# Kernel optimization log

Measured on AMD Instinct MI355X. Metric: run time of the kernel, lower is better.

Reference implementation:

```python
import jax, jax.numpy as jnp
import numpy as np


def setup_inputs() -> dict:
    key = jax.random.key(0)
    ks = jax.random.split(key, 6)
    B_, S, D_in, D_out, R, NH = 4, 2048, 4096, 4096, 16, 8
    return {
        "x": jax.random.normal(ks[0], (B_, S, D_in), dtype=jnp.float32),
        "W": jax.random.normal(ks[1], (D_out, D_in), dtype=jnp.float32) * 0.02,
        "b": jax.random.normal(ks[2], (D_out,), dtype=jnp.float32) * 0.02,
        "A": jax.random.normal(ks[3], (NH, R, D_in), dtype=jnp.float32) * 0.02,
        "H_mat": jax.random.normal(ks[4], (NH, R, R), dtype=jnp.float32) * 0.02,
        "B": jax.random.normal(ks[5], (NH, D_out, R), dtype=jnp.float32) * 0.02,
        "s": jnp.ones((NH,), dtype=jnp.float32),
    }


def reference(x, W, b, A, H_mat, B, s):
    # base linear: [B,S,D_out]
    out = jnp.einsum("bsd,od->bso", x, W) + b
    # batched low-rank adapter chain over heads h:
    # ax  = x @ A[h].T    : [B,h,S,r]
    ax = jnp.einsum("bsd,hrd->bhsr", x, A)
    # hax = ax @ H[h].T   : [B,h,S,r]
    hax = jnp.einsum("bhsr,hqr->bhsq", ax, H_mat)
    # accumulate s[h] * (hax @ B[h].T) into out
    out = out + jnp.einsum("h,bhsq,hoq->bso", s, hax, B)
    return out
```

## Files before the change

### kernel.cpp

```cpp
#include <hip/hip_runtime.h>
#include <hip/hip_bf16.h>

typedef __attribute__((ext_vector_type(4))) float f32x4;
typedef __attribute__((ext_vector_type(8))) short bf16x8;

#define M_DIM 8192
#define N_DIM 4096
#define K_DIM 4096
#define NH 8
#define R_DIM 16
#define HQ 128

__device__ __forceinline__ unsigned short f2bf(float f) {
  union { float f; unsigned int u; } v; v.f = f;
  unsigned int r = v.u + 0x7fffu + ((v.u >> 16) & 1u);
  return (unsigned short)(r >> 16);
}

__device__ __forceinline__ void gll16(const void* gptr, void* lptr) {
  __builtin_amdgcn_global_load_lds(
      (const __attribute__((address_space(1))) void*)gptr,
      (__attribute__((address_space(3))) void*)lptr, 16, 0, 0);
}

__device__ __forceinline__ unsigned lds_addr(const void* p) {
  return (unsigned)(uintptr_t)(const __attribute__((address_space(3))) void*)p;
}

#define FENCE() asm volatile("" ::: "memory")
#define BAR() do { FENCE(); __builtin_amdgcn_s_barrier(); FENCE(); } while (0)
#define LGKM(N) do { asm volatile("s_waitcnt lgkmcnt(" #N ")" ::: "memory"); \
  __builtin_amdgcn_sched_barrier(0); } while (0)
#define VMC(N) asm volatile("s_waitcnt vmcnt(" #N ")" ::: "memory")
#define DSR(D, ADDR, IMM) asm volatile("ds_read_b128 %0, %1 offset:%2" \
  : "=&v"(D) : "v"(ADDR), "i"(IMM))

__global__ void k_cast_bf16(const float* __restrict__ in,
                            unsigned short* __restrict__ out, int n4) {
  int i = blockIdx.x * 256 + threadIdx.x;
  if (i >= n4) return;
  float4 v = reinterpret_cast<const float4*>(in)[i];
  ushort4 o;
  o.x = f2bf(v.x); o.y = f2bf(v.y); o.z = f2bf(v.z); o.w = f2bf(v.w);
  reinterpret_cast<ushort4*>(out)[i] = o;
}

__global__ void k_ha_t(const float* __restrict__ A, const float* __restrict__ H,
                       const float* __restrict__ s, unsigned short* __restrict__ HA_T) {
  const int d = blockIdx.x * 256 + threadIdx.x;
  const int h = blockIdx.y;
  const float* Ah = A + (size_t)h * R_DIM * K_DIM;
  const float* Hh = H + h * R_DIM * R_DIM;
  const float sv = s[h];
  float acc[R_DIM];
  #pragma unroll
  for (int q = 0; q < R_DIM; ++q) acc[q] = 0.f;
  #pragma unroll
  for (int r = 0; r < R_DIM; ++r) {
    float a = Ah[(size_t)r * K_DIM + d];
    #pragma unroll
    for (int q = 0; q < R_DIM; ++q) acc[q] += Hh[q * R_DIM + r] * a;
  }
  unsigned short o[R_DIM];
  #pragma unroll
  for (int q = 0; q < R_DIM; ++q) o[q] = f2bf(acc[q] * sv);
  *reinterpret_cast<uint4*>(&HA_T[(size_t)d * HQ + h * R_DIM]) = *reinterpret_cast<uint4*>(o);
  *reinterpret_cast<uint4*>(&HA_T[(size_t)d * HQ + h * R_DIM + 8]) = *reinterpret_cast<uint4*>(o + 8);
}

__global__ void k_bcat(const float* __restrict__ Bm, unsigned short* __restrict__ Bc) {
  const int t = threadIdx.x;
  const int ol = t >> 4, q = t & 15;
  const int o = blockIdx.x * 16 + ol;
  #pragma unroll
  for (int h = 0; h < NH; ++h)
    Bc[(size_t)o * HQ + h * R_DIM + q] = f2bf(Bm[((size_t)h * N_DIM + o) * R_DIM + q]);
}

__global__ __launch_bounds__(256)
void k_weff_mfma(const unsigned short* __restrict__ Ab,
                 const unsigned short* __restrict__ Bb,
                 const float* __restrict__ W,
                 unsigned short* __restrict__ Weff) {
  constexpr int WK = HQ;
  __shared__ unsigned short As[128 * 32];
  __shared__ unsigned short Bs[128 * 32];

  const int t = threadIdx.x;
  const int lane = t & 63;
  const int wave = t >> 6;
  const int wr = wave >> 1, wc = wave & 1;
  const int brow = blockIdx.y * 128;
  const int bcol = blockIdx.x * 128;

  const int r0 = t >> 2, ch = t & 3;
  const size_t a_off0 = (size_t)(brow + r0) * WK + ch * 8;
  const size_t a_off1 = (size_t)(brow + r0 + 64) * WK + ch * 8;
  const size_t b_off0 = (size_t)(bcol + r0) * WK + ch * 8;
  const size_t b_off1 = (size_t)(bcol + r0 + 64) * WK + ch * 8;
  unsigned short* as_d0 = As + t * 8;
  unsigned short* as_d1 = As + (t + 256) * 8;
  unsigned short* bs_d0 = Bs + t * 8;
  unsigned short* bs_d1 = Bs + (t + 256) * 8;

  const int fr = lane & 15;
  const int kk = (lane >> 4) * 8;

  f32x4 acc[4][4] = {};

  for (int k0 = 0; k0 < WK; k0 += 32) {
    gll16(Ab + a_off0 + k0, as_d0);
    gll16(Ab + a_off1 + k0, as_d1);
    gll16(Bb + b_off0 + k0, bs_d0);
    gll16(Bb + b_off1 + k0, bs_d1);
    __syncthreads();

    bf16x8 af[4], bfr[4];
    #pragma unroll
    for (int m = 0; m < 4; ++m)
      af[m] = *reinterpret_cast<const bf16x8*>(&As[(wr * 64 + m * 16 + fr) * 32 + kk]);
    #pragma unroll
    for (int n = 0; n < 4; ++n)
      bfr[n] = *reinterpret_cast<const bf16x8*>(&Bs[(wc * 64 + n * 16 + fr) * 32 + kk]);

    #pragma unroll
    for (int m = 0; m < 4; ++m)
      #pragma unroll
      for (int n = 0; n < 4; ++n)
        acc[m][n] = __builtin_amdgcn_mfma_f32_16x16x32_bf16(af[m], bfr[n], acc[m][n], 0, 0, 0);

    __syncthreads();
  }

  const int crow0 = brow + wr * 64 + (lane >> 4) * 4;
  const int ccol0 = bcol + wc * 64 + fr;
  #pragma unroll
  for (int m = 0; m < 4; ++m)
    #pragma unroll
    for (int n = 0; n < 4; ++n) {
      const int col = ccol0 + n * 16;
      #pragma unroll
      for (int r = 0; r < 4; ++r) {
        const size_t idx = (size_t)(crow0 + m * 16 + r) * N_DIM + col;
        Weff[idx] = f2bf(acc[m][n][r] + W[idx]);
      }
    }
}

__global__ __launch_bounds__(512, 2)
void k_gemm256(const unsigned short* __restrict__ A,
               const unsigned short* __restrict__ Bw,
               const float* __restrict__ bias,
               float* __restrict__ C) {
  __shared__ unsigned short As[4][128][64];
  __shared__ unsigned short Bs[4][128][64];
  constexpr int SLOT_E = 128 * 64;

  const int t    = threadIdx.x;
  const int lane = t & 63;
  const int wave = t >> 6;
  const int wr   = wave >> 2;
  const int wc   = wave & 3;
  const int fr   = lane & 15;
  const int kq   = lane >> 4;

  const int bid = blockIdx.x;
  const int swz = (bid & 7) * 64 + (bid >> 3);
  const int brow = (swz >> 4) * 256;
  const int bcol = (swz & 15) * 256;

  const unsigned short* Ag = A  + (size_t)brow * K_DIM;
  const unsigned short* Bg = Bw + (size_t)bcol * K_DIM;

  const int i0 = t, i1 = 512 + t;
  const int r_s0 = i0 >> 3, r_s1 = i1 >> 3;
  const int c_e0 = (((i0 & 7) * 16) ^ ((r_s0 & 7) << 4)) >> 1;
  const int c_e1 = (((i1 & 7) * 16) ^ ((r_s1 & 7) << 4)) >> 1;

  unsigned short* as0 = &As[0][0][0];
  unsigned short* bs0 = &Bs[0][0][0];

  const int arow  = wr * 64 + fr;
  const int browl = wc * 32 + fr;
  const int axr   = (fr & 7) << 4;
  const unsigned colx0 = (unsigned)((kq * 16) ^ axr);
  const unsigned colx1 = (unsigned)((kq * 16 + 64) ^ axr);
  const unsigned aK0 = lds_addr(as0) + arow * 128 + colx0;
  const unsigned aK1 = lds_addr(as0) + arow * 128 + colx1;
  const unsigned bK0 = lds_addr(bs0) + browl * 128 + colx0;
  const unsigned bK1 = lds_addr(bs0) + browl * 128 + colx1;

#define STAGE(DST, GBASE, T_, H_) do { \
    gll16((GBASE) + (size_t)((H_) * 128 + r_s0) * K_DIM + (T_) * 64 + c_e0, (DST) + i0 * 8); \
    gll16((GBASE) + (size_t)((H_) * 128 + r_s1) * K_DIM + (T_) * 64 + c_e1, (DST) + i1 * 8); \
  } while (0)

#define RA_(AR, S) do { \
    DSR(AR[0][0], aK0, (S)*16384 + 0*2048); DSR(AR[0][1], aK1, (S)*16384 + 0*2048); \
    DSR(AR[1][0], aK0, (S)*16384 + 1*2048); DSR(AR[1][1], aK1, (S)*16384 + 1*2048); \
    DSR(AR[2][0], aK0, (S)*16384 + 2*2048); DSR(AR[2][1], aK1, (S)*16384 + 2*2048); \
    DSR(AR[3][0], aK0, (S)*16384 + 3*2048); DSR(AR[3][1], aK1, (S)*16384 + 3*2048); \
  } while (0)

#define RB_(BR, S) do { \
    DSR(BR[0][0], bK0, (S)*16384 + 0*2048); DSR(BR[0][1], bK1, (S)*16384 + 0*2048); \
    DSR(BR[1][0], bK0, (S)*16384 + 1*2048); DSR(BR[1][1], bK1, (S)*16384 + 1*2048); \
  } while (0)

#define QUAD(MH, NHX, AR, BR) do { \
    __builtin_amdgcn_s_setprio(1); \
    _Pragma("unroll") for (int m = 0; m < 4; ++m) \
    _Pragma("unroll") for (int n = 0; n < 2; ++n) \
    _Pragma("unroll") for (int ks = 0; ks < 2; ++ks) \
      acc[MH][NHX][m][n] = __builtin_amdgcn_mfma_f32_16x16x32_bf16(AR[m][ks], BR[n][ks], acc[MH][NHX][m][n], 0, 0, 0); \
    __builtin_amdgcn_s_setprio(0); \
  } while (0)

  bf16x8 arA[4][2], arB[4][2];
  bf16x8 bE[2][2],  bO[2][2];
  f32x4 acc[2][2][4][2] = {};

  STAGE(as0 + 0 * SLOT_E, Ag, 0, 0);
  STAGE(bs0 + 0 * SLOT_E, Bg, 0, 0);
  STAGE(bs0 + 1 * SLOT_E, Bg, 0, 1);
  STAGE(as0 + 1 * SLOT_E, Ag, 0, 1);
  STAGE(as0 + 2 * SLOT_E, Ag, 1, 0);
  STAGE(bs0 + 2 * SLOT_E, Bg, 1, 0);
  STAGE(bs0 + 3 * SLOT_E, Bg, 1, 1);
  VMC(6);
  BAR();

  #pragma unroll 1
  for (int it = 0; it < 31; ++it) {
    const int T = 2 * it;
    RA_(arA, 0); RB_(bE, 0); RB_(bO, 1);
    STAGE(as0 + 3 * SLOT_E, Ag, T + 1, 1);
    LGKM(4);  QUAD(0, 0, arA, bE);  BAR();
    RA_(arB, 1);
    STAGE(as0 + 0 * SLOT_E, Ag, T + 2, 0);
    LGKM(8);  QUAD(0, 1, arA, bO);  BAR();
    STAGE(bs0 + 0 * SLOT_E, Bg, T + 2, 0);
    LGKM(0);  QUAD(1, 0, arB, bE);  BAR();
    STAGE(bs0 + 1 * SLOT_E, Bg, T + 2, 1);
    QUAD(1, 1, arB, bO);
    VMC(6);
    BAR();
    RA_(arA, 2); RB_(bE, 2); RB_(bO, 3);
    STAGE(as0 + 1 * SLOT_E, Ag, T + 2, 1);
    LGKM(4);  QUAD(0, 0, arA, bE);  BAR();
    RA_(arB, 3);
    STAGE(as0 + 2 * SLOT_E, Ag, T + 3, 0);
    LGKM(8);  QUAD(0, 1, arA, bO);  BAR();
    STAGE(bs0 + 2 * SLOT_E, Bg, T + 3, 0);
    LGKM(0);  QUAD(1, 0, arB, bE);  BAR();
    STAGE(bs0 + 3 * SLOT_E, Bg, T + 3, 1);
    QUAD(1, 1, arB, bO);
    VMC(6);
    BAR();
  }

  STAGE(as0 + 3 * SLOT_E, Ag, 63, 1);
  VMC(0);
  BAR();
  RA_(arA, 0); RB_(bE, 0); RB_(bO, 1); LGKM(4);  QUAD(0, 0, arA, bE);
  RA_(arB, 1);                         LGKM(8);  QUAD(0, 1, arA, bO);
                                       LGKM(0);  QUAD(1, 0, arB, bE);
                                                 QUAD(1, 1, arB, bO);
  RA_(arA, 2); RB_(bE, 2); RB_(bO, 3); LGKM(4);  QUAD(0, 0, arA, bE);
  RA_(arB, 3);                         LGKM(8);  QUAD(0, 1, arA, bO);
                                       LGKM(0);  QUAD(1, 0, arB, bE);
                                                 QUAD(1, 1, arB, bO);

#undef STAGE
#undef RA_
#undef RB_
#undef QUAD

  const int crow = brow + wr * 64 + kq * 4;
  const int ccol = bcol + wc * 32 + fr;
  #pragma unroll
  for (int mh = 0; mh < 2; ++mh)
  #pragma unroll
  for (int nh = 0; nh < 2; ++nh)
  #pragma unroll
  for (int m = 0; m < 4; ++m)
  #pragma unroll
  for (int n = 0; n < 2; ++n) {
    const int col = ccol + nh * 128 + n * 16;
    const float bv = bias[col];
    #pragma unroll
    for (int r = 0; r < 4; ++r)
      C[(size_t)(crow + mh * 128 + m * 16 + r) * N_DIM + col] = acc[mh][nh][m][n][r] + bv;
  }
}

extern "C" void kernel_launch(void* const* d_in, const int* in_sizes, int n_in,
                              void* d_out, int out_size, void* d_ws, size_t ws_size,
                              hipStream_t stream) {
  const float* x  = (const float*)d_in[0];
  const float* W  = (const float*)d_in[1];
  const float* bv = (const float*)d_in[2];
  const float* Am = (const float*)d_in[3];
  const float* Hm = (const float*)d_in[4];
  const float* Bm = (const float*)d_in[5];
  const float* sv = (const float*)d_in[6];
  float* out = (float*)d_out;

  char* ws = (char*)d_ws;
  unsigned short* xbf  = (unsigned short*)ws;
  unsigned short* weff = (unsigned short*)(ws + (size_t)M_DIM * K_DIM * 2);
  unsigned short* hat  = (unsigned short*)(ws + (size_t)(M_DIM + N_DIM) * K_DIM * 2);
  unsigned short* bc   = (unsigned short*)(ws + (size_t)(M_DIM + N_DIM) * K_DIM * 2 + (size_t)N_DIM * HQ * 2);

  k_cast_bf16<<<(M_DIM * K_DIM / 4 + 255) / 256, 256, 0, stream>>>(x, xbf, M_DIM * K_DIM / 4);
  k_ha_t<<<dim3(K_DIM / 256, NH), 256, 0, stream>>>(Am, Hm, sv, hat);
  k_bcat<<<N_DIM / 16, 256, 0, stream>>>(Bm, bc);
  k_weff_mfma<<<dim3(N_DIM / 128, N_DIM / 128), 256, 0, stream>>>(bc, hat, W, weff);
  k_gemm256<<<dim3(512), 512, 0, stream>>>(xbf, weff, bv, out);
}
```

Measured before the change: 290.2 us.

## Prefetch next half-tile LDS fragments before final quadrant MFMA

Restructures the software pipeline so the LDS reads for the next K half-step (A fragments and B fragments) are issued before the last MFMA quadrant of the current half, rather than after the barrier at the top of each half. The odd B fragment is split into two double-buffered register sets so the new reads do not overwrite data still in use. The vmcnt waits are tightened and moved earlier. The aim is to hide LDS read latency behind MFMA work, at the cost of more registers and a more delicate barrier and wait ordering.

```diff
diff --git a/kernel.cpp b/kernel.cpp
--- a/kernel.cpp
+++ b/kernel.cpp
@@ -217,7 +217,8 @@
   } while (0)
 
   bf16x8 arA[4][2], arB[4][2];
-  bf16x8 bE[2][2],  bO[2][2];
+  bf16x8 bE[2][2];
+  bf16x8 bOe[2][2], bOo[2][2];
   f32x4 acc[2][2][4][2] = {};
 
   STAGE(as0 + 0 * SLOT_E, Ag, 0, 0);
@@ -229,47 +230,53 @@
   STAGE(bs0 + 3 * SLOT_E, Bg, 1, 1);
   VMC(6);
   BAR();
+  RA_(arA, 0); RB_(bE, 0); RB_(bOe, 1);
 
   #pragma unroll 1
   for (int it = 0; it < 31; ++it) {
     const int T = 2 * it;
-    RA_(arA, 0); RB_(bE, 0); RB_(bO, 1);
     STAGE(as0 + 3 * SLOT_E, Ag, T + 1, 1);
     LGKM(4);  QUAD(0, 0, arA, bE);  BAR();
     RA_(arB, 1);
     STAGE(as0 + 0 * SLOT_E, Ag, T + 2, 0);
-    LGKM(8);  QUAD(0, 1, arA, bO);  BAR();
+    LGKM(8);  QUAD(0, 1, arA, bOe);  BAR();
     STAGE(bs0 + 0 * SLOT_E, Bg, T + 2, 0);
-    LGKM(0);  QUAD(1, 0, arB, bE);  BAR();
+    LGKM(0);  QUAD(1, 0, arB, bE);
+    VMC(4);
+    BAR();
+    RA_(arA, 2); RB_(bE, 2); RB_(bOo, 3);
     STAGE(bs0 + 1 * SLOT_E, Bg, T + 2, 1);
-    QUAD(1, 1, arB, bO);
-    VMC(6);
+    QUAD(1, 1, arB, bOe);
     BAR();
-    RA_(arA, 2); RB_(bE, 2); RB_(bO, 3);
     STAGE(as0 + 1 * SLOT_E, Ag, T + 2, 1);
     LGKM(4);  QUAD(0, 0, arA, bE);  BAR();
     RA_(arB, 3);
     STAGE(as0 + 2 * SLOT_E, Ag, T + 3, 0);
-    LGKM(8);  QUAD(0, 1, arA, bO);  BAR();
+    LGKM(8);  QUAD(0, 1, arA, bOo);  BAR();
     STAGE(bs0 + 2 * SLOT_E, Bg, T + 3, 0);
-    LGKM(0);  QUAD(1, 0, arB, bE);  BAR();
+    LGKM(0);  QUAD(1, 0, arB, bE);
+    VMC(4);
+    BAR();
+    RA_(arA, 0); RB_(bE, 0); RB_(bOe, 1);
     STAGE(bs0 + 3 * SLOT_E, Bg, T + 3, 1);
-    QUAD(1, 1, arB, bO);
-    VMC(6);
+    QUAD(1, 1, arB, bOo);
     BAR();
   }
 
   STAGE(as0 + 3 * SLOT_E, Ag, 63, 1);
   VMC(0);
   BAR();
-  RA_(arA, 0); RB_(bE, 0); RB_(bO, 1); LGKM(4);  QUAD(0, 0, arA, bE);
-  RA_(arB, 1);                         LGKM(8);  QUAD(0, 1, arA, bO);
-                                       LGKM(0);  QUAD(1, 0, arB, bE);
-                                                 QUAD(1, 1, arB, bO);
-  RA_(arA, 2); RB_(bE, 2); RB_(bO, 3); LGKM(4);  QUAD(0, 0, arA, bE);
-  RA_(arB, 3);                         LGKM(8);  QUAD(0, 1, arA, bO);
-                                       LGKM(0);  QUAD(1, 0, arB, bE);
-                                                 QUAD(1, 1, arB, bO);
+  LGKM(4);  QUAD(0, 0, arA, bE);
+  RA_(arB, 1);
+  LGKM(8);  QUAD(0, 1, arA, bOe);
+  LGKM(0);  QUAD(1, 0, arB, bE);
+  RA_(arA, 2); RB_(bE, 2); RB_(bOo, 3);
+  QUAD(1, 1, arB, bOe);
+  LGKM(4);  QUAD(0, 0, arA, bE);
+  RA_(arB, 3);
+  LGKM(8);  QUAD(0, 1, arA, bOo);
+  LGKM(0);  QUAD(1, 0, arB, bE);
+  QUAD(1, 1, arB, bOo);
 
 #undef STAGE
 #undef RA_
```

Result: slower. 675.0 us (+132.6%).
